# Kernel optimization log

Measured on AMD Instinct MI355X. Metric: run time of the kernel, lower is better.

The kernel has to match this reference:

```python
import jax, jax.numpy as jnp
import numpy as np

B, N, Q, Z, C, L = 1, 6, 20000, 4, 128, 4
IMG_H, IMG_W = 256, 704
PC_RANGE = (-50.0, -50.0, -4.0, 50.0, 50.0, 4.0)
NUM_FREQS = 10
EPS = 1e-5
LEVEL_HW = ((64, 176), (32, 88), (16, 44), (8, 22))


def _mlp(x, ws, bs):
    for i, (w, b) in enumerate(zip(ws, bs)):
        x = x @ w + b
        if i < len(ws) - 1:
            x = jax.nn.relu(x)
    return x


def _bilinear(feat_hwc, px, py):
    # feat_hwc: [H, W, C]; px, py: [P] pixel coords. align_corners=False, zero padding.
    H, W, _ = feat_hwc.shape
    x0 = jnp.floor(px).astype(jnp.int32)
    y0 = jnp.floor(py).astype(jnp.int32)
    wx = px - x0
    wy = py - y0

    def gather(yi, xi):
        inb = ((yi >= 0) & (yi < H) & (xi >= 0) & (xi < W)).astype(feat_hwc.dtype)
        return feat_hwc[jnp.clip(yi, 0, H - 1), jnp.clip(xi, 0, W - 1)] * inb[:, None]

    return (gather(y0, x0) * ((1 - wy) * (1 - wx))[:, None]
          + gather(y0, x0 + 1) * ((1 - wy) * wx)[:, None]
          + gather(y0 + 1, x0) * (wy * (1 - wx))[:, None]
          + gather(y0 + 1, x0 + 1) * (wy * wx)[:, None])


def _pointbev_forward(feats, reference_points, lidar2img,
                      pe_w1, pe_b1, pe_w2, pe_b2, wt_w, wt_b, hm_ws, hm_bs):
    pos = jnp.transpose(reference_points, (0, 2, 1, 3))            # [B,Q,Z,3] in [0,1]
    # sinusoidal positional encoding map (normalized=False: coords used as-is)
    freqs = (2.0 ** jnp.arange(NUM_FREQS, dtype=pos.dtype)) * jnp.pi
    ang = pos[..., None] * freqs                                   # [B,Q,Z,3,F]
    pe_in = jnp.concatenate([jnp.sin(ang), jnp.cos(ang)], axis=-1)
    pe_in = pe_in.reshape(pos.shape[:-1] + (3 * 2 * NUM_FREQS,))
    pos_emb = _mlp(pe_in, [pe_w1, pe_w2], [pe_b1, pe_b2])          # [B,Q,Z,C]
    scale_w = jax.nn.softmax(pos_emb @ wt_w + wt_b, axis=-1)       # [B,Q,Z,L]

    # unnormalize to metric lidar coords via pc_range
    lo = jnp.asarray(PC_RANGE[:3], pos.dtype)
    span = jnp.asarray(PC_RANGE[3:], pos.dtype) - lo
    pts4 = jnp.concatenate([pos * span + lo, jnp.ones_like(pos[..., :1])], axis=-1)
    cam = jnp.einsum('bnij,bqzj->bnqzi', lidar2img, pts4)          # [B,N,Q,Z,4]
    homo = cam[..., 2]
    uv = cam[..., :2] / jnp.maximum(homo, EPS)[..., None]
    u = uv[..., 0] / IMG_W
    v = uv[..., 1] / IMG_H
    valid = ((homo > EPS) & (u > 0.0) & (u < 1.0) & (v > 0.0) & (v < 1.0)).astype(pos.dtype)

    sampler = jax.vmap(_bilinear)
    uf = u.reshape(B * N, Q * Z)
    vf = v.reshape(B * N, Q * Z)
    out = jnp.zeros((B, Q, Z, C), pos.dtype)
    for l, feat in enumerate(feats):                               # L=4 fixed levels
        Hl, Wl = feat.shape[2], feat.shape[3]
        s = sampler(feat.reshape(B * N, Hl, Wl, C), uf * Wl - 0.5, vf * Hl - 0.5)
        s = s.reshape(B, N, Q, Z, C) * valid[..., None]            # mask invalid projections
        out = out + s.sum(axis=1) * scale_w[..., l, None]          # sum views, weight level
    out = (out + pos_emb).reshape(B, Q, Z * C)
    return _mlp(out, hm_ws, hm_bs)                                 # [B,Q,C]


def setup_inputs():
    key = jax.random.key(0)
    ks = jax.random.split(key, 32)
    inp = {}
    for l, (h, w) in enumerate(LEVEL_HW):
        inp[f"feat{l}"] = jax.random.normal(ks[l], (B, N, h, w, C), jnp.float32)
    inp["reference_points"] = jax.random.uniform(ks[8], (B, Z, Q, 3), jnp.float32)
    # structured nuScenes-like lidar2img = intrinsics @ extrinsics for a 6-camera ring
    l2i = np.zeros((B, N, 4, 4), np.float32)
    K = np.array([[400.0, 0.0, IMG_W / 2, 0.0],
                  [0.0, 400.0, IMG_H / 2, 0.0],
                  [0.0, 0.0, 1.0, 0.0],
                  [0.0, 0.0, 0.0, 1.0]], np.float32)
    for n in range(N):
        yaw = 2.0 * np.pi * n / N
        cy, sy = np.cos(yaw), np.sin(yaw)
        R = np.array([[-sy, cy, 0.0], [0.0, 0.0, -1.0], [cy, sy, 0.0]], np.float32)
        E = np.eye(4, dtype=np.float32)
        E[:3, :3] = R
        E[:3, 3] = [0.0, 1.5, 0.5]
        l2i[0, n] = K @ E
    inp["lidar2img"] = jnp.asarray(l2i)

    def lin(k, fi, fo):
        s = 1.0 / np.sqrt(fi)
        return jax.random.uniform(k, (fi, fo), jnp.float32, -s, s)

    d_in = 3 * 2 * NUM_FREQS
    inp["pe_w1"] = lin(ks[9], d_in, 2 * C); inp["pe_b1"] = jnp.zeros((2 * C,), jnp.float32)
    inp["pe_w2"] = lin(ks[10], 2 * C, C);   inp["pe_b2"] = jnp.zeros((C,), jnp.float32)
    inp["wt_w"] = lin(ks[11], C, L);        inp["wt_b"] = jnp.zeros((L,), jnp.float32)
    dims = [Z * C, 2 * Z * C, 2 * Z * C, 2 * Z * C, C]
    for i in range(4):
        inp[f"hm_w{i+1}"] = lin(ks[12 + i], dims[i], dims[i + 1])
        inp[f"hm_b{i+1}"] = jnp.zeros((dims[i + 1],), jnp.float32)
    return inp


def reference(feat0, feat1, feat2, feat3, reference_points, lidar2img,
              pe_w1, pe_b1, pe_w2, pe_b2, wt_w, wt_b,
              hm_w1, hm_b1, hm_w2, hm_b2, hm_w3, hm_b3, hm_w4, hm_b4):
    return _pointbev_forward((feat0, feat1, feat2, feat3), reference_points, lidar2img,
                             pe_w1, pe_b1, pe_w2, pe_b2, wt_w, wt_b,
                             [hm_w1, hm_w2, hm_w3, hm_w4], [hm_b1, hm_b2, hm_b3, hm_b4])
```

## Files before the change

kernel.cpp:

```cpp
#include <hip/hip_runtime.h>
#include <math.h>

#define QN 20000
#define PN 80000
#define CN 128
#define NVIEW 6

typedef __attribute__((ext_vector_type(8))) _Float16 h8;
typedef __attribute__((ext_vector_type(4))) _Float16 h4;
typedef __attribute__((ext_vector_type(4))) float f32x4;

__device__ __forceinline__ void gload16(const void* g, void* l) {
  __builtin_amdgcn_global_load_lds(
      (const __attribute__((address_space(1))) void*)g,
      (__attribute__((address_space(3))) void*)l, 16, 0, 0);
}

__global__ __launch_bounds__(256) void wtrans_all(
    const float* __restrict__ w0, const float* __restrict__ w1,
    const float* __restrict__ w2, const float* __restrict__ w3,
    const float* __restrict__ w4, const float* __restrict__ w5,
    _Float16* __restrict__ base) {
  __shared__ float t[32][33];
  int b = blockIdx.x;
  const float* W; _Float16* T; int K, N, Kp, nbx, lb;
  if (b < 16)        { W = w0; T = base + 0;       K = 60;   N = 256;  Kp = 64;   nbx = 8;  lb = b; }
  else if (b < 48)   { W = w1; T = base + 32768;   K = 256;  N = 128;  Kp = 256;  nbx = 4;  lb = b - 16; }
  else if (b < 560)  { W = w2; T = base + 98304;   K = 512;  N = 1024; Kp = 512;  nbx = 32; lb = b - 48; }
  else if (b < 1584) { W = w3; T = base + 1146880; K = 1024; N = 1024; Kp = 1024; nbx = 32; lb = b - 560; }
  else if (b < 2608) { W = w4; T = base + 3244032; K = 1024; N = 1024; Kp = 1024; nbx = 32; lb = b - 1584; }
  else               { W = w5; T = base + 5341184; K = 1024; N = 128;  Kp = 1024; nbx = 4;  lb = b - 2608; }
  const int n0 = (lb % nbx) * 32, k0 = (lb / nbx) * 32;
  const int tx = threadIdx.x & 31, ty = threadIdx.x >> 5;
  #pragma unroll
  for (int j = 0; j < 4; ++j) {
    int k = k0 + ty + j * 8;
    t[ty + j * 8][tx] = (k < K) ? W[(size_t)k * N + n0 + tx] : 0.f;
  }
  __syncthreads();
  #pragma unroll
  for (int j = 0; j < 4; ++j) {
    int n = n0 + ty + j * 8;
    int k = k0 + tx;
    T[(size_t)n * Kp + k] = (_Float16)t[tx][ty + j * 8];
  }
}

__global__ __launch_bounds__(256) void fcvt_kernel(
    const float* __restrict__ s0, const float* __restrict__ s1,
    const float* __restrict__ s2, const float* __restrict__ s3,
    _Float16* __restrict__ d) {
  size_t i = (size_t)blockIdx.x * 256 + threadIdx.x;
  if (i >= 2872320) return;
  const float* s; size_t off;
  if (i < 2162688)      { s = s0; off = 0; }
  else if (i < 2703360) { s = s1; off = 2162688; }
  else if (i < 2838528) { s = s2; off = 2703360; }
  else                  { s = s3; off = 2838528; }
  f32x4 v = *(const f32x4*)(s + (i - off) * 4);
  h4 o;
  o[0] = (_Float16)v[0]; o[1] = (_Float16)v[1];
  o[2] = (_Float16)v[2]; o[3] = (_Float16)v[3];
  *(h4*)(d + i * 4) = o;
}

__global__ __launch_bounds__(256) void pe_in_kernel(const float* __restrict__ rp,
                                                    _Float16* __restrict__ P) {
  int idx = blockIdx.x * 256 + threadIdx.x;
  if (idx >= PN * 64) return;
  int p = idx >> 6, k = idx & 63;
  float val = 0.f;
  if (k < 60) {
    int q = p >> 2, z = p & 3;
    int d = k / 20, r = k - d * 20;
    int j = (r >= 10) ? (r - 10) : r;
    float pos = rp[((size_t)z * QN + q) * 3 + d];
    float ang = pos * ((float)(1 << j) * 3.14159265358979323846f);
    val = (r >= 10) ? cosf(ang) : sinf(ang);
  }
  P[idx] = (_Float16)val;
}

__global__ __launch_bounds__(256) void lw_kernel(const _Float16* __restrict__ posE,
                                                 const float* __restrict__ wtw,
                                                 const float* __restrict__ wtb,
                                                 float* __restrict__ lw) {
  __shared__ float swtT[512];
  __shared__ float sb[4];
  const int tid = threadIdx.x;
  for (int i = tid; i < 512; i += 256) swtT[(i & 3) * 128 + (i >> 2)] = wtw[i];
  if (tid < 4) sb[tid] = wtb[tid];
  __syncthreads();

  const int wave = tid >> 6, lane = tid & 63;
  const int grp = lane >> 4, s = lane & 15;
  const int p = blockIdx.x * 16 + wave * 4 + grp;
  const int c0 = s * 8;
  h8 pa = *(const h8*)(posE + (size_t)p * CN + c0);

  float lg[4];
  #pragma unroll
  for (int l = 0; l < 4; ++l) {
    const float* w = swtT + l * 128 + c0;
    float acc = 0.f;
    #pragma unroll
    for (int j = 0; j < 8; ++j) acc = fmaf((float)pa[j], w[j], acc);
    lg[l] = acc;
  }
  #pragma unroll
  for (int off = 8; off > 0; off >>= 1) {
    lg[0] += __shfl_xor(lg[0], off);
    lg[1] += __shfl_xor(lg[1], off);
    lg[2] += __shfl_xor(lg[2], off);
    lg[3] += __shfl_xor(lg[3], off);
  }
  lg[0] += sb[0]; lg[1] += sb[1]; lg[2] += sb[2]; lg[3] += sb[3];
  float mx = fmaxf(fmaxf(lg[0], lg[1]), fmaxf(lg[2], lg[3]));
  float e0 = __expf(lg[0] - mx), e1 = __expf(lg[1] - mx);
  float e2 = __expf(lg[2] - mx), e3 = __expf(lg[3] - mx);
  float esr = 1.f / (e0 + e1 + e2 + e3);
  if (s == 0) {
    f32x4 o = {e0 * esr, e1 * esr, e2 * esr, e3 * esr};
    *(f32x4*)(lw + (size_t)p * 4) = o;
  }
}

template <bool RELU, int OUT>
__global__ __launch_bounds__(256, 4) void gemm_h(const _Float16* __restrict__ A,
                                                 const _Float16* __restrict__ B,
                                                 const float* __restrict__ bias,
                                                 float* __restrict__ Cf,
                                                 _Float16* __restrict__ Ch,
                                                 int M, int N, int K,
                                                 int nbn) {
  __shared__ _Float16 sm[2][2][4096];
  const int tid = threadIdx.x;
  const int wave = tid >> 6, lane = tid & 63;
  const int wr = wave >> 1, wc = wave & 1;
  const int g = lane >> 4, r16 = lane & 15;

  const int nwg = gridDim.x;
  const int q8 = nwg >> 3, r8 = nwg & 7;
  const int xcd = blockIdx.x & 7, sub = blockIdx.x >> 3;
  const int wg = (xcd < r8 ? xcd * (q8 + 1) : r8 * (q8 + 1) + (xcd - r8) * q8) + sub;
  const int bn = (wg % nbn) * 128;
  const int bm = (wg / nbn) * 128;
  const int nt = K >> 5;

  f32x4 acc[4][4];
  #pragma unroll
  for (int i = 0; i < 4; ++i)
    #pragma unroll
    for (int j = 0; j < 4; ++j) acc[i][j] = {0.f, 0.f, 0.f, 0.f};

  auto STAGE = [&](int buf, int t) {
    const int kof = t << 5;
    const int rsub = lane >> 2;
    const int slot0 = lane & 3;
    #pragma unroll
    for (int pl = 0; pl < 2; ++pl) {
      const _Float16* P = (pl == 0) ? A : B;
      const int rbase = (pl == 0) ? bm : bn;
      #pragma unroll
      for (int i = 0; i < 2; ++i) {
        int group = wave * 2 + i;
        int row = group * 16 + rsub;
        int slot = slot0 ^ ((row >> 1) & 3);
        int gr = rbase + row;
        if (pl == 0 && gr >= M) gr = M - 1;
        gload16(P + (size_t)gr * K + kof + slot * 8,
                &sm[buf][pl][group * 512]);
      }
    }
  };

  auto COMPUTE = [&](int buf) {
    h8 a[4], b[4];
    #pragma unroll
    for (int mi = 0; mi < 4; ++mi) {
      int row = wr * 64 + mi * 16 + r16;
      int off = row * 32 + ((g ^ ((row >> 1) & 3)) * 8);
      a[mi] = *(const h8*)&sm[buf][0][off];
    }
    #pragma unroll
    for (int ni = 0; ni < 4; ++ni) {
      int row = wc * 64 + ni * 16 + r16;
      int off = row * 32 + ((g ^ ((row >> 1) & 3)) * 8);
      b[ni] = *(const h8*)&sm[buf][1][off];
    }
    #pragma unroll
    for (int mi = 0; mi < 4; ++mi)
      #pragma unroll
      for (int ni = 0; ni < 4; ++ni)
        acc[mi][ni] = __builtin_amdgcn_mfma_f32_16x16x32_f16(a[mi], b[ni], acc[mi][ni], 0, 0, 0);
  };

  STAGE(0, 0);
  __syncthreads();

  for (int t = 0; t < nt; ++t) {
    if (t + 1 < nt) STAGE((t + 1) & 1, t + 1);
    COMPUTE(t & 1);
    __syncthreads();
  }

  #pragma unroll
  for (int mi = 0; mi < 4; ++mi) {
    int gr0 = bm + wr * 64 + mi * 16 + (lane >> 4) * 4;
    #pragma unroll
    for (int ni = 0; ni < 4; ++ni) {
      int gc = bn + wc * 64 + ni * 16 + r16;
      float bv = bias[gc];
      #pragma unroll
      for (int r = 0; r < 4; ++r) {
        int row = gr0 + r;
        if (row >= M) continue;
        float v = acc[mi][ni][r] + bv;
        if (RELU) v = fmaxf(v, 0.f);
        if (OUT == 0) Cf[(size_t)row * N + gc] = v;
        else          Ch[(size_t)row * N + gc] = (_Float16)v;
      }
    }
  }
}

template <bool RELU, int OUT>
__global__ __launch_bounds__(128, 3) void gemm_h64(const _Float16* __restrict__ A,
                                                   const _Float16* __restrict__ B,
                                                   const float* __restrict__ bias,
                                                   float* __restrict__ Cf,
                                                   _Float16* __restrict__ Ch,
                                                   int M, int N, int K,
                                                   int nbn) {
  __shared__ _Float16 smA[2][64 * 32];
  __shared__ _Float16 smB[2][128 * 32];
  const int tid = threadIdx.x;
  const int wave = tid >> 6, lane = tid & 63;
  const int wc = wave;
  const int g = lane >> 4, r16 = lane & 15;

  const int nwg = gridDim.x;
  const int q8 = nwg >> 3, r8 = nwg & 7;
  const int xcd = blockIdx.x & 7, sub = blockIdx.x >> 3;
  const int wg = (xcd < r8 ? xcd * (q8 + 1) : r8 * (q8 + 1) + (xcd - r8) * q8) + sub;
  const int bn = (wg % nbn) * 128;
  const int bm = (wg / nbn) * 64;
  const int nt = K >> 5;

  f32x4 acc[4][4];
  #pragma unroll
  for (int i = 0; i < 4; ++i)
    #pragma unroll
    for (int j = 0; j < 4; ++j) acc[i][j] = {0.f, 0.f, 0.f, 0.f};

  auto STAGE = [&](int buf, int t) {
    const int kof = t << 5;
    const int rsub = lane >> 2;
    const int slot0 = lane & 3;
    #pragma unroll
    for (int i = 0; i < 2; ++i) {
      int group = wave * 2 + i;
      int row = group * 16 + rsub;
      int slot = slot0 ^ ((row >> 1) & 3);
      int gr = bm + row; if (gr >= M) gr = M - 1;
      gload16(A + (size_t)gr * K + kof + slot * 8, &smA[buf][group * 512]);
    }
    #pragma unroll
    for (int i = 0; i < 4; ++i) {
      int group = wave * 4 + i;
      int row = group * 16 + rsub;
      int slot = slot0 ^ ((row >> 1) & 3);
      gload16(B + (size_t)(bn + row) * K + kof + slot * 8, &smB[buf][group * 512]);
    }
  };

  auto COMPUTE = [&](int buf) {
    h8 a[4], b[4];
    #pragma unroll
    for (int mi = 0; mi < 4; ++mi) {
      int row = mi * 16 + r16;
      int off = row * 32 + ((g ^ ((row >> 1) & 3)) * 8);
      a[mi] = *(const h8*)&smA[buf][off];
    }
    #pragma unroll
    for (int ni = 0; ni < 4; ++ni) {
      int row = wc * 64 + ni * 16 + r16;
      int off = row * 32 + ((g ^ ((row >> 1) & 3)) * 8);
      b[ni] = *(const h8*)&smB[buf][off];
    }
    #pragma unroll
    for (int mi = 0; mi < 4; ++mi)
      #pragma unroll
      for (int ni = 0; ni < 4; ++ni)
        acc[mi][ni] = __builtin_amdgcn_mfma_f32_16x16x32_f16(a[mi], b[ni], acc[mi][ni], 0, 0, 0);
  };

  STAGE(0, 0);
  __syncthreads();

  for (int t = 0; t < nt; ++t) {
    if (t + 1 < nt) STAGE((t + 1) & 1, t + 1);
    COMPUTE(t & 1);
    __syncthreads();
  }

  #pragma unroll
  for (int mi = 0; mi < 4; ++mi) {
    int gr0 = bm + mi * 16 + (lane >> 4) * 4;
    #pragma unroll
    for (int ni = 0; ni < 4; ++ni) {
      int gc = bn + wc * 64 + ni * 16 + r16;
      float bv = bias[gc];
      #pragma unroll
      for (int r = 0; r < 4; ++r) {
        int row = gr0 + r;
        if (row >= M) continue;
        float v = acc[mi][ni][r] + bv;
        if (RELU) v = fmaxf(v, 0.f);
        if (OUT == 0) Cf[(size_t)row * N + gc] = v;
        else          Ch[(size_t)row * N + gc] = (_Float16)v;
      }
    }
  }
}

__global__ __launch_bounds__(256) void sample_kernel(
    const _Float16* __restrict__ fbase,
    const float* __restrict__ rp, const float* __restrict__ l2i,
    const float* __restrict__ lw,
    const _Float16* __restrict__ posE, _Float16* __restrict__ X0) {
  __shared__ float sl2i[96];
  const int tid = threadIdx.x;
  if (tid < 96) sl2i[tid] = l2i[tid];
  __syncthreads();

  const _Float16* FL[4] = {fbase, fbase + 8650752, fbase + 10813440,
                           fbase + 11354112};

  const int wave = tid >> 6, lane = tid & 63;
  const int half = lane >> 5, s = lane & 31;
  const int p = blockIdx.x * 8 + wave * 2 + half;
  const int q = p >> 2, z = p & 3;

  const float X  = rp[((size_t)z * QN + q) * 3 + 0] * 100.f - 50.f;
  const float Y  = rp[((size_t)z * QN + q) * 3 + 1] * 100.f - 50.f;
  const float Zc = rp[((size_t)z * QN + q) * 3 + 2] * 8.f - 4.f;

  const int c0 = s * 4;
  h4 pa = *(const h4*)(posE + (size_t)p * CN + c0);
  const float pe0 = (float)pa[0], pe1 = (float)pa[1];
  const float pe2 = (float)pa[2], pe3 = (float)pa[3];

  f32x4 lw4 = *(const f32x4*)(lw + (size_t)p * 4);
  float swl[4] = {lw4[0], lw4[1], lw4[2], lw4[3]};

  float a0 = 0.f, a1 = 0.f, a2 = 0.f, a3 = 0.f;
  for (int n = 0; n < NVIEW; n++) {
    const float* Mx = sl2i + n * 16;
    float cam0 = Mx[0] * X + Mx[1] * Y + Mx[2]  * Zc + Mx[3];
    float cam1 = Mx[4] * X + Mx[5] * Y + Mx[6]  * Zc + Mx[7];
    float cam2 = Mx[8] * X + Mx[9] * Y + Mx[10] * Zc + Mx[11];
    float denom = fmaxf(cam2, 1e-5f);
    float u = cam0 / denom * (1.f / 704.f);
    float v = cam1 / denom * (1.f / 256.f);
    bool valid = (cam2 > 1e-5f) & (u > 0.f) & (u < 1.f) & (v > 0.f) & (v < 1.f);
    if (!valid) continue;
    float px3 = u * 22.f - 0.5f, py3 = v * 8.f - 0.5f;
    bool interior = (px3 >= 0.f) & (py3 >= 0.f) & (px3 < 21.f) & (py3 < 7.f);
    if (interior) {
      #pragma unroll
      for (int l = 0; l < 4; l++) {
        const int Hl = 64 >> l, Wl = 176 >> l;
        float pxl = u * (float)Wl - 0.5f;
        float pyl = v * (float)Hl - 0.5f;
        float fx = floorf(pxl), fy = floorf(pyl);
        int x0 = (int)fx, y0 = (int)fy;
        float wx = pxl - fx, wy = pyl - fy;
        float w1r = wy * swl[l], w0r = swl[l] - w1r;
        float w01 = w0r * wx, w00 = w0r - w01;
        float w11 = w1r * wx, w10 = w1r - w11;
        const _Float16* cp = FL[l]
            + ((size_t)n * (Hl * Wl) + (size_t)(y0 * Wl + x0)) * CN + c0;
        h4 v00 = *(const h4*)(cp);
        h4 v01 = *(const h4*)(cp + CN);
        h4 v10 = *(const h4*)(cp + Wl * CN);
        h4 v11 = *(const h4*)(cp + Wl * CN + CN);
        a0 = fmaf(w00, (float)v00[0], fmaf(w01, (float)v01[0], fmaf(w10, (float)v10[0], fmaf(w11, (float)v11[0], a0))));
        a1 = fmaf(w00, (float)v00[1], fmaf(w01, (float)v01[1], fmaf(w10, (float)v10[1], fmaf(w11, (float)v11[1], a1))));
        a2 = fmaf(w00, (float)v00[2], fmaf(w01, (float)v01[2], fmaf(w10, (float)v10[2], fmaf(w11, (float)v11[2], a2))));
        a3 = fmaf(w00, (float)v00[3], fmaf(w01, (float)v01[3], fmaf(w10, (float)v10[3], fmaf(w11, (float)v11[3], a3))));
      }
    } else {
      #pragma unroll
      for (int l = 0; l < 4; l++) {
        const int Hl = 64 >> l, Wl = 176 >> l;
        float pxl = u * (float)Wl - 0.5f;
        float pyl = v * (float)Hl - 0.5f;
        float fx = floorf(pxl), fy = floorf(pyl);
        int x0 = (int)fx, y0 = (int)fy;
        float wx = pxl - fx, wy = pyl - fy;
        float w1r = wy * swl[l], w0r = swl[l] - w1r;
        const float wxs[2] = {1.f - wx, wx};
        const float wrs[2] = {w0r, w1r};
        const _Float16* fb = FL[l] + (size_t)n * (Hl * Wl) * CN;
        #pragma unroll
        for (int cy = 0; cy < 2; cy++) {
          #pragma unroll
          for (int cx = 0; cx < 2; cx++) {
            int xi = x0 + cx, yi = y0 + cy;
            bool inb = ((unsigned)xi < (unsigned)Wl) & ((unsigned)yi < (unsigned)Hl);
            int off = inb ? (yi * Wl + xi) * CN : 0;
            float wgt = inb ? (wrs[cy] * wxs[cx]) : 0.f;
            h4 vv = *(const h4*)(fb + off + c0);
            a0 = fmaf(wgt, (float)vv[0], a0);
            a1 = fmaf(wgt, (float)vv[1], a1);
            a2 = fmaf(wgt, (float)vv[2], a2);
            a3 = fmaf(wgt, (float)vv[3], a3);
          }
        }
      }
    }
  }
  h4 o;
  o[0] = (_Float16)(a0 + pe0);
  o[1] = (_Float16)(a1 + pe1);
  o[2] = (_Float16)(a2 + pe2);
  o[3] = (_Float16)(a3 + pe3);
  *(h4*)&X0[(size_t)p * CN + c0] = o;
}

extern "C" void kernel_launch(void* const* d_in, const int* in_sizes, int n_in,
                              void* d_out, int out_size, void* d_ws, size_t ws_size,
                              hipStream_t stream) {
  const float* feat0 = (const float*)d_in[0];
  const float* feat1 = (const float*)d_in[1];
  const float* feat2 = (const float*)d_in[2];
  const float* feat3 = (const float*)d_in[3];
  const float* rp    = (const float*)d_in[4];
  const float* l2i   = (const float*)d_in[5];
  const float* pe_w1 = (const float*)d_in[6];
  const float* pe_b1 = (const float*)d_in[7];
  const float* pe_w2 = (const float*)d_in[8];
  const float* pe_b2 = (const float*)d_in[9];
  const float* wt_w  = (const float*)d_in[10];
  const float* wt_b  = (const float*)d_in[11];
  const float* hm_w1 = (const float*)d_in[12];
  const float* hm_b1 = (const float*)d_in[13];
  const float* hm_w2 = (const float*)d_in[14];
  const float* hm_b2 = (const float*)d_in[15];
  const float* hm_w3 = (const float*)d_in[16];
  const float* hm_b3 = (const float*)d_in[17];
  const float* hm_w4 = (const float*)d_in[18];
  const float* hm_b4 = (const float*)d_in[19];
  float* out = (float*)d_out;

  char* ws = (char*)d_ws;
  typedef _Float16 h16;
  h16* wPE1 = (h16*)(ws + 0);
  h16* wPE2 = (h16*)(ws + 65536);
  h16* wH1  = (h16*)(ws + 196608);
  h16* wH2  = (h16*)(ws + 2293760);
  h16* wH3  = (h16*)(ws + 6488064);
  h16* wH4  = (h16*)(ws + 10682368);

  h16*   posE = (h16*)(ws + 11534336);
  float* lwga = (float*)(ws + 33000000);
  h16*   hpe  = (h16*)(ws + 53000192);
  h16*   pein = (h16*)(ws + 94000128);
  h16*   X0   = (h16*)(ws + 53000192);
  h16*   H1   = (h16*)(ws + 94000128);
  h16*   H2   = (h16*)(ws + 11534336);
  h16*   H3   = (h16*)(ws + 94000128);
  h16*   f16b = (h16*)(ws + 136000000);

  wtrans_all<<<2736, 256, 0, stream>>>(pe_w1, pe_w2, hm_w1, hm_w2, hm_w3, hm_w4,
                                       (h16*)ws);
  fcvt_kernel<<<(2872320 + 255) / 256, 256, 0, stream>>>(feat0, feat1, feat2,
                                                         feat3, f16b);

  pe_in_kernel<<<(PN * 64 + 255) / 256, 256, 0, stream>>>(rp, pein);

  gemm_h<true, 1><<<2 * 625, 256, 0, stream>>>(pein, wPE1, pe_b1, nullptr, hpe, PN, 256, 64, 2);
  gemm_h64<false, 1><<<1250, 128, 0, stream>>>(hpe, wPE2, pe_b2, nullptr, posE, PN, 128, 256, 1);

  lw_kernel<<<PN / 16, 256, 0, stream>>>(posE, wt_w, wt_b, lwga);

  sample_kernel<<<PN / 8, 256, 0, stream>>>(f16b, rp, l2i, lwga, posE, X0);

  gemm_h<true, 1><<<8 * 157, 256, 0, stream>>>(X0, wH1, hm_b1, nullptr, H1, QN, 1024, 512, 8);
  gemm_h<true, 1><<<8 * 157, 256, 0, stream>>>(H1, wH2, hm_b2, nullptr, H2, QN, 1024, 1024, 8);
  gemm_h<true, 1><<<8 * 157, 256, 0, stream>>>(H2, wH3, hm_b3, nullptr, H3, QN, 1024, 1024, 8);
  gemm_h64<false, 0><<<313, 128, 0, stream>>>(H3, wH4, hm_b4, out, nullptr, QN, 128, 1024, 1);
}
```

Before: 322.6 us.

## Merge prep kernels, add 128x256 GEMM tile with finer waits, retile small GEMMs

Folds the weight transpose, feature fp16 conversion and PE-input generation into one launch to cut launch overhead. Replaces the 64x128 GEMM with a 256-thread 128x256 tile for the three big head-MLP layers, using explicit vmcnt/lgkmcnt waits instead of full __syncthreads to overlap loads and compute. The small-N GEMMs switch to the existing gemm_h kernel. Larger tiles give more reuse but fewer blocks (628) and higher register pressure, and the hand-written waitcnt values must match the number of outstanding loads.

```diff
diff --git a/kernel.cpp b/kernel.cpp
--- a/kernel.cpp
+++ b/kernel.cpp
@@ -16,69 +16,65 @@
       (__attribute__((address_space(3))) void*)l, 16, 0, 0);
 }
 
-__global__ __launch_bounds__(256) void wtrans_all(
+__global__ __launch_bounds__(256) void prep_all(
     const float* __restrict__ w0, const float* __restrict__ w1,
     const float* __restrict__ w2, const float* __restrict__ w3,
     const float* __restrict__ w4, const float* __restrict__ w5,
-    _Float16* __restrict__ base) {
-  __shared__ float t[32][33];
-  int b = blockIdx.x;
-  const float* W; _Float16* T; int K, N, Kp, nbx, lb;
-  if (b < 16)        { W = w0; T = base + 0;       K = 60;   N = 256;  Kp = 64;   nbx = 8;  lb = b; }
-  else if (b < 48)   { W = w1; T = base + 32768;   K = 256;  N = 128;  Kp = 256;  nbx = 4;  lb = b - 16; }
-  else if (b < 560)  { W = w2; T = base + 98304;   K = 512;  N = 1024; Kp = 512;  nbx = 32; lb = b - 48; }
-  else if (b < 1584) { W = w3; T = base + 1146880; K = 1024; N = 1024; Kp = 1024; nbx = 32; lb = b - 560; }
-  else if (b < 2608) { W = w4; T = base + 3244032; K = 1024; N = 1024; Kp = 1024; nbx = 32; lb = b - 1584; }
-  else               { W = w5; T = base + 5341184; K = 1024; N = 128;  Kp = 1024; nbx = 4;  lb = b - 2608; }
-  const int n0 = (lb % nbx) * 32, k0 = (lb / nbx) * 32;
-  const int tx = threadIdx.x & 31, ty = threadIdx.x >> 5;
-  #pragma unroll
-  for (int j = 0; j < 4; ++j) {
-    int k = k0 + ty + j * 8;
-    t[ty + j * 8][tx] = (k < K) ? W[(size_t)k * N + n0 + tx] : 0.f;
-  }
-  __syncthreads();
-  #pragma unroll
-  for (int j = 0; j < 4; ++j) {
-    int n = n0 + ty + j * 8;
-    int k = k0 + tx;
-    T[(size_t)n * Kp + k] = (_Float16)t[tx][ty + j * 8];
-  }
-}
-
-__global__ __launch_bounds__(256) void fcvt_kernel(
+    _Float16* __restrict__ wbase,
     const float* __restrict__ s0, const float* __restrict__ s1,
     const float* __restrict__ s2, const float* __restrict__ s3,
-    _Float16* __restrict__ d) {
-  size_t i = (size_t)blockIdx.x * 256 + threadIdx.x;
-  if (i >= 2872320) return;
-  const float* s; size_t off;
-  if (i < 2162688)      { s = s0; off = 0; }
-  else if (i < 2703360) { s = s1; off = 2162688; }
-  else if (i < 2838528) { s = s2; off = 2703360; }
-  else                  { s = s3; off = 2838528; }
-  f32x4 v = *(const f32x4*)(s + (i - off) * 4);
-  h4 o;
-  o[0] = (_Float16)v[0]; o[1] = (_Float16)v[1];
-  o[2] = (_Float16)v[2]; o[3] = (_Float16)v[3];
-  *(h4*)(d + i * 4) = o;
-}
-
-__global__ __launch_bounds__(256) void pe_in_kernel(const float* __restrict__ rp,
-                                                    _Float16* __restrict__ P) {
-  int idx = blockIdx.x * 256 + threadIdx.x;
-  if (idx >= PN * 64) return;
-  int p = idx >> 6, k = idx & 63;
-  float val = 0.f;
-  if (k < 60) {
-    int q = p >> 2, z = p & 3;
-    int d = k / 20, r = k - d * 20;
-    int j = (r >= 10) ? (r - 10) : r;
-    float pos = rp[((size_t)z * QN + q) * 3 + d];
-    float ang = pos * ((float)(1 << j) * 3.14159265358979323846f);
-    val = (r >= 10) ? cosf(ang) : sinf(ang);
-  }
-  P[idx] = (_Float16)val;
+    _Float16* __restrict__ fdst,
+    const float* __restrict__ rp, _Float16* __restrict__ pedst) {
+  int b = blockIdx.x;
+  if (b < 2736) {
+    __shared__ float t[32][33];
+    const float* W; _Float16* T; int K, N, Kp, nbx, lb;
+    if (b < 16)        { W = w0; T = wbase + 0;       K = 60;   N = 256;  Kp = 64;   nbx = 8;  lb = b; }
+    else if (b < 48)   { W = w1; T = wbase + 32768;   K = 256;  N = 128;  Kp = 256;  nbx = 4;  lb = b - 16; }
+    else if (b < 560)  { W = w2; T = wbase + 98304;   K = 512;  N = 1024; Kp = 512;  nbx = 32; lb = b - 48; }
+    else if (b < 1584) { W = w3; T = wbase + 1146880; K = 1024; N = 1024; Kp = 1024; nbx = 32; lb = b - 560; }
+    else if (b < 2608) { W = w4; T = wbase + 3244032; K = 1024; N = 1024; Kp = 1024; nbx = 32; lb = b - 1584; }
+    else               { W = w5; T = wbase + 5341184; K = 1024; N = 128;  Kp = 1024; nbx = 4;  lb = b - 2608; }
+    const int n0 = (lb % nbx) * 32, k0 = (lb / nbx) * 32;
+    const int tx = threadIdx.x & 31, ty = threadIdx.x >> 5;
+    #pragma unroll
+    for (int j = 0; j < 4; ++j) {
+      int k = k0 + ty + j * 8;
+      t[ty + j * 8][tx] = (k < K) ? W[(size_t)k * N + n0 + tx] : 0.f;
+    }
+    __syncthreads();
+    #pragma unroll
+    for (int j = 0; j < 4; ++j) {
+      int n = n0 + ty + j * 8;
+      int k = k0 + tx;
+      T[(size_t)n * Kp + k] = (_Float16)t[tx][ty + j * 8];
+    }
+  } else if (b < 13956) {
+    size_t i = (size_t)(b - 2736) * 256 + threadIdx.x;
+    const float* s; size_t off;
+    if (i < 2162688)      { s = s0; off = 0; }
+    else if (i < 2703360) { s = s1; off = 2162688; }
+    else if (i < 2838528) { s = s2; off = 2703360; }
+    else                  { s = s3; off = 2838528; }
+    f32x4 v = *(const f32x4*)(s + (i - off) * 4);
+    h4 o;
+    o[0] = (_Float16)v[0]; o[1] = (_Float16)v[1];
+    o[2] = (_Float16)v[2]; o[3] = (_Float16)v[3];
+    *(h4*)(fdst + i * 4) = o;
+  } else {
+    int idx = (b - 13956) * 256 + threadIdx.x;
+    int p = idx >> 6, k = idx & 63;
+    float val = 0.f;
+    if (k < 60) {
+      int q = p >> 2, z = p & 3;
+      int d = k / 20, r = k - d * 20;
+      int j = (r >= 10) ? (r - 10) : r;
+      float pos = rp[((size_t)z * QN + q) * 3 + d];
+      float ang = pos * ((float)(1 << j) * 3.14159265358979323846f);
+      val = (r >= 10) ? cosf(ang) : sinf(ang);
+    }
+    pedst[idx] = (_Float16)val;
+  }
 }
 
 __global__ __launch_bounds__(256) void lw_kernel(const _Float16* __restrict__ posE,
@@ -225,15 +221,15 @@
 }
 
 template <bool RELU, int OUT>
-__global__ __launch_bounds__(128, 3) void gemm_h64(const _Float16* __restrict__ A,
-                                                   const _Float16* __restrict__ B,
-                                                   const float* __restrict__ bias,
-                                                   float* __restrict__ Cf,
-                                                   _Float16* __restrict__ Ch,
-                                                   int M, int N, int K,
-                                                   int nbn) {
-  __shared__ _Float16 smA[2][64 * 32];
-  __shared__ _Float16 smB[2][128 * 32];
+__global__ __launch_bounds__(256, 2) void gemm_h256(const _Float16* __restrict__ A,
+                                                    const _Float16* __restrict__ B,
+                                                    const float* __restrict__ bias,
+                                                    float* __restrict__ Cf,
+                                                    _Float16* __restrict__ Ch,
+                                                    int M, int N, int K,
+                                                    int nbn) {
+  __shared__ _Float16 smA[2][128 * 32];
+  __shared__ _Float16 smB[2][256 * 32];
   const int tid = threadIdx.x;
   const int wave = tid >> 6, lane = tid & 63;
   const int wc = wave;
@@ -243,13 +239,13 @@
   const int q8 = nwg >> 3, r8 = nwg & 7;
   const int xcd = blockIdx.x & 7, sub = blockIdx.x >> 3;
   const int wg = (xcd < r8 ? xcd * (q8 + 1) : r8 * (q8 + 1) + (xcd - r8) * q8) + sub;
-  const int bn = (wg % nbn) * 128;
-  const int bm = (wg / nbn) * 64;
+  const int bn = (wg % nbn) * 256;
+  const int bm = (wg / nbn) * 128;
   const int nt = K >> 5;
 
-  f32x4 acc[4][4];
-  #pragma unroll
-  for (int i = 0; i < 4; ++i)
+  f32x4 acc[8][4];
+  #pragma unroll
+  for (int i = 0; i < 8; ++i)
     #pragma unroll
     for (int j = 0; j < 4; ++j) acc[i][j] = {0.f, 0.f, 0.f, 0.f};
 
@@ -275,13 +271,7 @@
   };
 
   auto COMPUTE = [&](int buf) {
-    h8 a[4], b[4];
-    #pragma unroll
-    for (int mi = 0; mi < 4; ++mi) {
-      int row = mi * 16 + r16;
-      int off = row * 32 + ((g ^ ((row >> 1) & 3)) * 8);
-      a[mi] = *(const h8*)&smA[buf][off];
-    }
+    h8 b[4];
     #pragma unroll
     for (int ni = 0; ni < 4; ++ni) {
       int row = wc * 64 + ni * 16 + r16;
@@ -289,23 +279,34 @@
       b[ni] = *(const h8*)&smB[buf][off];
     }
     #pragma unroll
-    for (int mi = 0; mi < 4; ++mi)
+    for (int mi = 0; mi < 8; ++mi) {
+      int row = mi * 16 + r16;
+      int off = row * 32 + ((g ^ ((row >> 1) & 3)) * 8);
+      h8 a = *(const h8*)&smA[buf][off];
       #pragma unroll
       for (int ni = 0; ni < 4; ++ni)
-        acc[mi][ni] = __builtin_amdgcn_mfma_f32_16x16x32_f16(a[mi], b[ni], acc[mi][ni], 0, 0, 0);
+        acc[mi][ni] = __builtin_amdgcn_mfma_f32_16x16x32_f16(a, b[ni], acc[mi][ni], 0, 0, 0);
+    }
   };
 
   STAGE(0, 0);
-  __syncthreads();
+  asm volatile("" ::: "memory");
 
   for (int t = 0; t < nt; ++t) {
-    if (t + 1 < nt) STAGE((t + 1) & 1, t + 1);
-    COMPUTE(t & 1);
-    __syncthreads();
-  }
-
-  #pragma unroll
-  for (int mi = 0; mi < 4; ++mi) {
+    const int cur = t & 1;
+    if (t + 1 < nt) {
+      STAGE(cur ^ 1, t + 1);
+      asm volatile("" ::: "memory");
+      asm volatile("s_waitcnt vmcnt(6)\n\ts_barrier" ::: "memory");
+    } else {
+      asm volatile("s_waitcnt vmcnt(0)\n\ts_barrier" ::: "memory");
+    }
+    COMPUTE(cur);
+    asm volatile("s_waitcnt lgkmcnt(0)\n\ts_barrier" ::: "memory");
+  }
+
+  #pragma unroll
+  for (int mi = 0; mi < 8; ++mi) {
     int gr0 = bm + mi * 16 + (lane >> 4) * 4;
     #pragma unroll
     for (int ni = 0; ni < 4; ++ni) {
@@ -473,22 +474,19 @@
   h16*   H3   = (h16*)(ws + 94000128);
   h16*   f16b = (h16*)(ws + 136000000);
 
-  wtrans_all<<<2736, 256, 0, stream>>>(pe_w1, pe_w2, hm_w1, hm_w2, hm_w3, hm_w4,
-                                       (h16*)ws);
-  fcvt_kernel<<<(2872320 + 255) / 256, 256, 0, stream>>>(feat0, feat1, feat2,
-                                                         feat3, f16b);
-
-  pe_in_kernel<<<(PN * 64 + 255) / 256, 256, 0, stream>>>(rp, pein);
+  prep_all<<<33956, 256, 0, stream>>>(pe_w1, pe_w2, hm_w1, hm_w2, hm_w3, hm_w4,
+                                      (h16*)ws, feat0, feat1, feat2, feat3,
+                                      f16b, rp, pein);
 
   gemm_h<true, 1><<<2 * 625, 256, 0, stream>>>(pein, wPE1, pe_b1, nullptr, hpe, PN, 256, 64, 2);
-  gemm_h64<false, 1><<<1250, 128, 0, stream>>>(hpe, wPE2, pe_b2, nullptr, posE, PN, 128, 256, 1);
+  gemm_h<false, 1><<<1 * 625, 256, 0, stream>>>(hpe, wPE2, pe_b2, nullptr, posE, PN, 128, 256, 1);
 
   lw_kernel<<<PN / 16, 256, 0, stream>>>(posE, wt_w, wt_b, lwga);
 
   sample_kernel<<<PN / 8, 256, 0, stream>>>(f16b, rp, l2i, lwga, posE, X0);
 
-  gemm_h<true, 1><<<8 * 157, 256, 0, stream>>>(X0, wH1, hm_b1, nullptr, H1, QN, 1024, 512, 8);
-  gemm_h<true, 1><<<8 * 157, 256, 0, stream>>>(H1, wH2, hm_b2, nullptr, H2, QN, 1024, 1024, 8);
-  gemm_h<true, 1><<<8 * 157, 256, 0, stream>>>(H2, wH3, hm_b3, nullptr, H3, QN, 1024, 1024, 8);
-  gemm_h64<false, 0><<<313, 128, 0, stream>>>(H3, wH4, hm_b4, out, nullptr, QN, 128, 1024, 1);
-}
+  gemm_h256<true, 1><<<4 * 157, 256, 0, stream>>>(X0, wH1, hm_b1, nullptr, H1, QN, 1024, 512, 4);
+  gemm_h256<true, 1><<<4 * 157, 256, 0, stream>>>(H1, wH2, hm_b2, nullptr, H2, QN, 1024, 1024, 4);
+  gemm_h256<true, 1><<<4 * 157, 256, 0, stream>>>(H2, wH3, hm_b3, nullptr, H3, QN, 1024, 1024, 4);
+  gemm_h<false, 0><<<1 * 157, 256, 0, stream>>>(H3, wH4, hm_b4, out, nullptr, QN, 128, 1024, 1);
+}
```

Measured after the change: 397.9 us. 23.3% more time.
